# Performance work log

Measured on AMD Instinct MI355X. Metric: run time of the kernel, lower is better.

## Reference

```python
import jax, jax.numpy as jnp
import numpy as np

B, T, D = 64, 256, 512   # batch, seq_len, input_dim (= emb_dim)
HA = 512                 # alpha_dim
HB = 512                 # beta_dim (must equal alpha_dim due to source bug)
ODE = 256                # ode_dim


def _lin(key, out_d, in_d, scale):
    k1, k2 = jax.random.split(key)
    W = jax.random.uniform(k1, (out_d, in_d), jnp.float32, -scale, scale)
    b = jax.random.uniform(k2, (out_d,), jnp.float32, -scale, scale)
    return W, b


def setup_inputs() -> dict:
    key = jax.random.key(0)
    ks = jax.random.split(key, 16)
    x = jax.random.normal(ks[0], (B, T, D), jnp.float32)
    W_emb, b_emb = _lin(ks[1], D, D, 1.0 / np.sqrt(D))
    # LSTMCell params: gates order i, f, g, o ; shapes (4H, in) / (4H, H)
    sA = 1.0 / np.sqrt(HA)
    Wih_a = jax.random.uniform(ks[2], (4 * HA, D), jnp.float32, -sA, sA)
    Whh_a = jax.random.uniform(ks[3], (4 * HA, HA), jnp.float32, -sA, sA)
    bih_a = jax.random.uniform(ks[4], (4 * HA,), jnp.float32, -sA, sA)
    bhh_a = jax.random.uniform(ks[5], (4 * HA,), jnp.float32, -sA, sA)
    sB = 1.0 / np.sqrt(HB)
    Wih_b = jax.random.uniform(ks[6], (4 * HB, D), jnp.float32, -sB, sB)
    Whh_b = jax.random.uniform(ks[7], (4 * HB, HB), jnp.float32, -sB, sB)
    bih_b = jax.random.uniform(ks[8], (4 * HB,), jnp.float32, -sB, sB)
    bhh_b = jax.random.uniform(ks[9], (4 * HB,), jnp.float32, -sB, sB)
    W_aatt, b_aatt = _lin(ks[10], 1, HA, 1.0 / np.sqrt(HA))
    W_batt, b_batt = _lin(ks[11], D, HB, 1.0 / np.sqrt(HB))
    W_mu, b_mu = _lin(ks[12], ODE, D, 1.0 / np.sqrt(D))
    W_sig, b_sig = _lin(ks[13], ODE, D, 1.0 / np.sqrt(D))
    ah0 = jax.random.normal(ks[14], (B, HA), jnp.float32)
    k15a, k15b, k15c = jax.random.split(ks[15], 3)
    ac0 = jax.random.normal(k15a, (B, HA), jnp.float32)
    bh0 = jax.random.normal(k15b, (B, HB), jnp.float32)
    bc0 = jax.random.normal(k15c, (B, HB), jnp.float32)
    return dict(x=x, W_emb=W_emb, b_emb=b_emb,
                Wih_a=Wih_a, Whh_a=Whh_a, bih_a=bih_a, bhh_a=bhh_a,
                Wih_b=Wih_b, Whh_b=Whh_b, bih_b=bih_b, bhh_b=bhh_b,
                W_aatt=W_aatt, b_aatt=b_aatt, W_batt=W_batt, b_batt=b_batt,
                W_mu=W_mu, b_mu=b_mu, W_sig=W_sig, b_sig=b_sig,
                ah0=ah0, ac0=ac0, bh0=bh0, bc0=bc0)


def _lstm_scan(xs, h0, c0, Wih, Whh, bih, bhh):
    # xs: (T, B, D) -> (hs (T,B,H), hT (B,H))
    def step(carry, xt):
        h, c = carry
        g = xt @ Wih.T + bih + h @ Whh.T + bhh
        i, f, gg, o = jnp.split(g, 4, axis=-1)
        c = jax.nn.sigmoid(f) * c + jax.nn.sigmoid(i) * jnp.tanh(gg)
        h = jax.nn.sigmoid(o) * jnp.tanh(c)
        return (h, c), h
    (hT, _), hs = jax.lax.scan(step, (h0, c0), xs)
    return hs, hT


def reference(x, W_emb, b_emb, Wih_a, Whh_a, bih_a, bhh_a,
              Wih_b, Whh_b, bih_b, bhh_b, W_aatt, b_aatt,
              W_batt, b_batt, W_mu, b_mu, W_sig, b_sig,
              ah0, ac0, bh0, bc0):
    emb = x @ W_emb.T + b_emb                      # (B, T, D)
    rev = jnp.flip(emb.transpose(1, 0, 2), 0)      # (T, B, D) reversed time
    hs_a, hT_a = _lstm_scan(rev, ah0, ac0, Wih_a, Whh_a, bih_a, bhh_a)
    hi = jnp.flip(hs_a, 0).transpose(1, 0, 2)      # (B, T, HA)
    alpha = jax.nn.softmax(hi @ W_aatt.T + b_aatt, axis=1)  # (B, T, 1)
    # Faithful to source bug: beta loop appends the FINAL alpha_hx each step,
    # so gi is hT_a broadcast over time (beta LSTM output is discarded).
    _ = _lstm_scan(rev, bh0, bc0, Wih_b, Whh_b, bih_b, bhh_b)  # dead compute, DCE'd
    gi = jnp.broadcast_to(hT_a[:, None, :], (x.shape[0], x.shape[1], hT_a.shape[-1]))
    beta = jnp.tanh(gi @ W_batt.T + b_batt)        # (B, T, D)
    w = alpha * beta * emb                          # (B, T, D)
    var = jnp.sum(w, axis=1)                        # (B, D)
    mean = jnp.mean(w, axis=1)                      # (B, D)
    mu = mean @ W_mu.T + b_mu                       # (B, ODE)
    sigma = var @ W_sig.T + b_sig                   # (B, ODE)
    return (mu, sigma)
```

## Files before the change

### kernel.cpp

```cpp
#include <hip/hip_runtime.h>
#include <hip/hip_bf16.h>
#include <math.h>

#define BB_ 64
#define TT_ 256
#define DD_ 512
#define HH_ 512
#define G4_ 2048
#define ODE_ 256

#define NBLK_ 512

__device__ __forceinline__ float2 cohload2(const float* p) {
    unsigned long long u = __hip_atomic_load(
        (unsigned long long*)p, __ATOMIC_RELAXED, __HIP_MEMORY_SCOPE_AGENT);
    union { unsigned long long u; float2 f; } c; c.u = u;
    return c.f;
}
__device__ __forceinline__ void cohstore2(float* p, float a, float b) {
    union { unsigned long long u; float2 f; } c; c.f = make_float2(a, b);
    __hip_atomic_store((unsigned long long*)p, c.u,
                       __ATOMIC_RELAXED, __HIP_MEMORY_SCOPE_AGENT);
}

__device__ __forceinline__ float fsigmoid(float x) {
    return 1.f / (1.f + __expf(-x));
}
__device__ __forceinline__ float ftanh(float x) {
    float e = __expf(-2.f * fabsf(x));
    float t = (1.f - e) / (1.f + e);
    return copysignf(t, x);
}

template <int CTRL>
__device__ __forceinline__ float dpp_ror_add(float x) {
    int y = __builtin_amdgcn_update_dpp(0, __float_as_int(x), CTRL, 0xf, 0xf, false);
    return x + __int_as_float(y);
}
__device__ __forceinline__ float row16_allreduce(float x) {
    x = dpp_ror_add<0x121>(x);
    x = dpp_ror_add<0x122>(x);
    x = dpp_ror_add<0x124>(x);
    x = dpp_ror_add<0x128>(x);
    return x;
}

template <int ACT>
__global__ __launch_bounds__(256) void gemm_bt(
    const float* __restrict__ A, const float* __restrict__ W,
    const float* __restrict__ bias1, const float* __restrict__ bias2,
    float* __restrict__ C, int M, int N, int K, float scale)
{
    const int BM = 128, BN = 128, BK = 16;
    __shared__ float As[BK][BM + 4];
    __shared__ float Ws[BK][BN + 4];
    const int tid = threadIdx.x;
    const int tx = tid & 15, ty = tid >> 4;
    const int m0 = blockIdx.y * BM, n0 = blockIdx.x * BN;

    float acc[8][8];
#pragma unroll
    for (int i = 0; i < 8; ++i)
#pragma unroll
        for (int j = 0; j < 8; ++j) acc[i][j] = 0.f;

    int r0_ = (tid * 4) >> 4,        c0_ = (tid * 4) & 15;
    int r1_ = ((256 + tid) * 4) >> 4, c1_ = ((256 + tid) * 4) & 15;
    int gm0 = m0 + r0_; if (gm0 > M - 1) gm0 = M - 1;
    int gm1 = m0 + r1_; if (gm1 > M - 1) gm1 = M - 1;

    float4 pa0 = *(const float4*)(A + (size_t)gm0 * K + c0_);
    float4 pw0 = *(const float4*)(W + (size_t)(n0 + r0_) * K + c0_);
    float4 pa1 = *(const float4*)(A + (size_t)gm1 * K + c1_);
    float4 pw1 = *(const float4*)(W + (size_t)(n0 + r1_) * K + c1_);

    for (int k0 = 0; k0 < K; k0 += BK) {
        As[c0_ + 0][r0_] = pa0.x; As[c0_ + 1][r0_] = pa0.y;
        As[c0_ + 2][r0_] = pa0.z; As[c0_ + 3][r0_] = pa0.w;
        Ws[c0_ + 0][r0_] = pw0.x; Ws[c0_ + 1][r0_] = pw0.y;
        Ws[c0_ + 2][r0_] = pw0.z; Ws[c0_ + 3][r0_] = pw0.w;
        As[c1_ + 0][r1_] = pa1.x; As[c1_ + 1][r1_] = pa1.y;
        As[c1_ + 2][r1_] = pa1.z; As[c1_ + 3][r1_] = pa1.w;
        Ws[c1_ + 0][r1_] = pw1.x; Ws[c1_ + 1][r1_] = pw1.y;
        Ws[c1_ + 2][r1_] = pw1.z; Ws[c1_ + 3][r1_] = pw1.w;
        __syncthreads();

        if (k0 + BK < K) {
            int kn = k0 + BK;
            pa0 = *(const float4*)(A + (size_t)gm0 * K + kn + c0_);
            pw0 = *(const float4*)(W + (size_t)(n0 + r0_) * K + kn + c0_);
            pa1 = *(const float4*)(A + (size_t)gm1 * K + kn + c1_);
            pw1 = *(const float4*)(W + (size_t)(n0 + r1_) * K + kn + c1_);
        }

#pragma unroll
        for (int k = 0; k < BK; ++k) {
            float a[8], w[8];
#pragma unroll
            for (int i = 0; i < 8; ++i) a[i] = As[k][ty * 8 + i];
#pragma unroll
            for (int j = 0; j < 8; ++j) w[j] = Ws[k][tx * 8 + j];
#pragma unroll
            for (int i = 0; i < 8; ++i)
#pragma unroll
                for (int j = 0; j < 8; ++j) acc[i][j] += a[i] * w[j];
        }
        __syncthreads();
    }

#pragma unroll
    for (int j = 0; j < 8; ++j) {
        int n = n0 + tx * 8 + j;
        float bsum = bias1[n] + (bias2 ? bias2[n] : 0.f);
#pragma unroll
        for (int i = 0; i < 8; ++i) {
            int m = m0 + ty * 8 + i;
            if (m < M) {
                float v = acc[i][j] * scale + bsum;
                if (ACT == 1) v = tanhf(v);
                C[(size_t)m * N + n] = v;
            }
        }
    }
}

__global__ __launch_bounds__(256, 2) void lstm_persist(
    const float* __restrict__ gx,
    const float* __restrict__ Whh,
    const float* __restrict__ ac0,
    float* __restrict__ hT0,
    float* __restrict__ hT1,
    float* __restrict__ hsT,
    unsigned* __restrict__ cnt)
{
    __shared__ float h_s[512 * 12];
    __shared__ float gx_s[4 * 65];

    const int tid = threadIdx.x;
    const int bg = blockIdx.x >> 5;
    const int jb = blockIdx.x & 31;
    const int jh0 = jb * 16;
    const int b0  = bg * 4;
    const int kq   = tid & 15;
    const int jh_l = tid >> 4;
    const int jh   = jh0 + jh_l;

    float creg = 0.f;
    if (kq < 4) creg = ac0[(size_t)(b0 + kq) * HH_ + jh];

    float4 wreg[32];
#pragma unroll
    for (int kk = 0; kk < 32; ++kk) {
        int k = kk * 16 + kq;
        wreg[kk].x = Whh[(size_t)(0 * 512 + jh) * 512 + k];
        wreg[kk].y = Whh[(size_t)(1 * 512 + jh) * 512 + k];
        wreg[kk].z = Whh[(size_t)(2 * 512 + jh) * 512 + k];
        wreg[kk].w = Whh[(size_t)(3 * 512 + jh) * 512 + k];
    }

    const int g_lb = tid >> 6;
    const int g_g  = (tid >> 4) & 3;
    const int g_jl = tid & 15;
    const float* gsrc = gx + (size_t)(b0 + g_lb) * TT_ * G4_ + g_g * 512 + jh0 + g_jl;

    float gxreg = gsrc[(size_t)255 * G4_];

    for (int t = 0; t < TT_; ++t) {
        const float* hin = ((t & 1) ? hT1 : hT0) + (size_t)bg * 2048;
        float* hout      = ((t & 1) ? hT0 : hT1) + (size_t)bg * 2048;

        gx_s[g_lb * 65 + g_g * 16 + g_jl] = gxreg;

        float4 hstg[2];
#pragma unroll
        for (int w = 0; w < 2; ++w) {
            int c = w * 256 + tid;
            float2 a  = cohload2(hin + (size_t)c * 4);
            float2 b2 = cohload2(hin + (size_t)c * 4 + 2);
            hstg[w] = make_float4(a.x, a.y, b2.x, b2.y);
        }
#pragma unroll
        for (int w = 0; w < 2; ++w) {
            int c = w * 256 + tid;
            *(float4*)(h_s + (size_t)c * 12) = hstg[w];
        }
        __syncthreads();

        if (t + 1 < TT_)
            gxreg = gsrc[(size_t)(TT_ - 2 - t) * G4_];

        float acc[4][4];
#pragma unroll
        for (int i = 0; i < 4; ++i)
#pragma unroll
            for (int j = 0; j < 4; ++j) acc[i][j] = 0.f;

#pragma unroll
        for (int kk = 0; kk < 32; ++kk) {
            int k = kk * 16 + kq;
            float4 wv = wreg[kk];
            float4 ha = *(const float4*)(h_s + (size_t)k * 12);
            float hv[4] = {ha.x, ha.y, ha.z, ha.w};
#pragma unroll
            for (int bb = 0; bb < 4; ++bb) {
                acc[bb][0] += hv[bb] * wv.x;
                acc[bb][1] += hv[bb] * wv.y;
                acc[bb][2] += hv[bb] * wv.z;
                acc[bb][3] += hv[bb] * wv.w;
            }
        }

#pragma unroll
        for (int bb = 0; bb < 4; ++bb)
#pragma unroll
            for (int g = 0; g < 4; ++g)
                acc[bb][g] = row16_allreduce(acc[bb][g]);

        float hn = 0.f;
        if (kq < 4) {
            float gi = 0.f, gf = 0.f, gg = 0.f, go = 0.f;
#pragma unroll
            for (int bb = 0; bb < 4; ++bb)
                if (kq == bb) { gi = acc[bb][0]; gf = acc[bb][1];
                                gg = acc[bb][2]; go = acc[bb][3]; }
            gi += gx_s[kq * 65 + 0 * 16 + jh_l];
            gf += gx_s[kq * 65 + 1 * 16 + jh_l];
            gg += gx_s[kq * 65 + 2 * 16 + jh_l];
            go += gx_s[kq * 65 + 3 * 16 + jh_l];
            float si = fsigmoid(gi);
            float sf = fsigmoid(gf);
            float sg = ftanh(gg);
            float so = fsigmoid(go);
            creg = sf * creg + si * sg;
            hn = so * ftanh(creg);
        }
        float hn_up = __shfl_down(hn, 1);
        const bool do_st = (kq < 4) && ((kq & 1) == 0);
        if (do_st)
            cohstore2(hout + (size_t)jh * 4 + kq, hn, hn_up);

        __syncthreads();
        if (tid == 0)
            __hip_atomic_fetch_add(&cnt[(size_t)bg * 32], 1u,
                                   __ATOMIC_RELAXED, __HIP_MEMORY_SCOPE_AGENT);
        if (do_st)
            *(float2*)(hsT + ((size_t)t * 512 + jh) * 64 + b0 + kq) = make_float2(hn, hn_up);
        if (tid == 0) {
            unsigned tgt = (unsigned)(t + 1) * 32u;
            while (__hip_atomic_load(&cnt[(size_t)bg * 32],
                        __ATOMIC_RELAXED, __HIP_MEMORY_SCOPE_AGENT) < tgt)
                __builtin_amdgcn_s_sleep(1);
        }
        __syncthreads();
    }
}

__global__ __launch_bounds__(256) void h0_transpose(
    const float* __restrict__ ah0, float* __restrict__ hT0)
{
    int idx = blockIdx.x * 256 + threadIdx.x;
    int b = idx >> 9, jh = idx & 511;
    hT0[(size_t)(b >> 2) * 2048 + jh * 4 + (b & 3)] = ah0[idx];
}

__global__ __launch_bounds__(256) void att_scores_T(
    const float* __restrict__ hsT, const float* __restrict__ Wa,
    const float* __restrict__ ba, float* __restrict__ scores)
{
    int ts = blockIdx.x;
    int b = threadIdx.x & 63, part = threadIdx.x >> 6;
    const float* hp = hsT + (size_t)ts * 512 * 64;
    float s = 0.f;
#pragma unroll 8
    for (int jj = 0; jj < 128; ++jj) {
        int jh = part * 128 + jj;
        s += hp[(size_t)jh * 64 + b] * Wa[jh];
    }
    __shared__ float red[4][64];
    red[part][b] = s;
    __syncthreads();
    if (part == 0) {
        float tot = red[0][b] + red[1][b] + red[2][b] + red[3][b] + ba[0];
        scores[b * TT_ + (TT_ - 1 - ts)] = tot;
    }
}

__global__ __launch_bounds__(256) void softmax_wsum(
    const float* __restrict__ scores, const float* __restrict__ emb,
    float* __restrict__ s)
{
    const int b = blockIdx.x;
    const int tid = threadIdx.x;
    __shared__ float sm[256];
    __shared__ float red[16];
    float v = scores[b * TT_ + tid];
    float m = v;
#pragma unroll
    for (int off = 32; off; off >>= 1) m = fmaxf(m, __shfl_xor(m, off));
    int wv = tid >> 6, ln = tid & 63;
    if (ln == 0) red[wv] = m;
    __syncthreads();
    float bm = fmaxf(fmaxf(red[0], red[1]), fmaxf(red[2], red[3]));
    float e = expf(v - bm);
    float ss = e;
#pragma unroll
    for (int off = 32; off; off >>= 1) ss += __shfl_xor(ss, off);
    if (ln == 0) red[8 + wv] = ss;
    __syncthreads();
    float tot = red[8] + red[9] + red[10] + red[11];
    sm[tid] = e / tot;
    __syncthreads();

    float acc0 = 0.f, acc1 = 0.f;
    const float* ep = emb + (size_t)b * TT_ * DD_;
    for (int t = 0; t < TT_; ++t) {
        float a = sm[t];
        acc0 += a * ep[t * DD_ + tid];
        acc1 += a * ep[t * DD_ + 256 + tid];
    }
    s[b * DD_ + tid] = acc0;
    s[b * DD_ + 256 + tid] = acc1;
}

__global__ __launch_bounds__(256) void beta_from_hT(
    const float* __restrict__ hTT, const float* __restrict__ Wb,
    const float* __restrict__ bbias, float* __restrict__ beta)
{
    int b = threadIdx.x & 63, w = threadIdx.x >> 6;
    int d = blockIdx.x * 4 + w;
    const float* wrow = Wb + (size_t)d * 512;
    const float* hb = hTT + (size_t)(b >> 2) * 2048 + (b & 3);
    float s = 0.f;
#pragma unroll 8
    for (int jh = 0; jh < 512; ++jh)
        s += hb[(size_t)jh * 4] * wrow[jh];
    beta[(size_t)b * 512 + d] = tanhf(s + bbias[d]);
}

__global__ __launch_bounds__(256) void mulvec(
    const float* __restrict__ a, const float* __restrict__ b,
    float* __restrict__ o, int n)
{
    int i = blockIdx.x * 256 + threadIdx.x;
    if (i < n) o[i] = a[i] * b[i];
}

extern "C" void kernel_launch(void* const* d_in, const int* in_sizes, int n_in,
                              void* d_out, int out_size, void* d_ws, size_t ws_size,
                              hipStream_t stream) {
    const float* x      = (const float*)d_in[0];
    const float* W_emb  = (const float*)d_in[1];
    const float* b_emb  = (const float*)d_in[2];
    const float* Wih_a  = (const float*)d_in[3];
    const float* Whh_a  = (const float*)d_in[4];
    const float* bih_a  = (const float*)d_in[5];
    const float* bhh_a  = (const float*)d_in[6];
    const float* W_aatt = (const float*)d_in[11];
    const float* b_aatt = (const float*)d_in[12];
    const float* W_batt = (const float*)d_in[13];
    const float* b_batt = (const float*)d_in[14];
    const float* W_mu   = (const float*)d_in[15];
    const float* b_mu   = (const float*)d_in[16];
    const float* W_sig  = (const float*)d_in[17];
    const float* b_sig  = (const float*)d_in[18];
    const float* ah0    = (const float*)d_in[19];
    const float* ac0    = (const float*)d_in[20];

    const size_t N_EMB = (size_t)BB_ * TT_ * DD_;
    const size_t N_GX  = (size_t)BB_ * TT_ * G4_;
    const size_t N_HS  = (size_t)TT_ * HH_ * BB_;
    const size_t N_BH  = (size_t)BB_ * HH_;
    const size_t N_BAR = 8192;

    size_t need_floats = N_BAR + N_EMB + N_GX + N_HS + 2 * N_BH
                       + (size_t)BB_ * TT_ + 3 * N_BH;
    if (ws_size < need_floats * sizeof(float)) return;

    float* ws     = (float*)d_ws;
    unsigned* cnt = (unsigned*)d_ws;
    float* emb    = ws + N_BAR;
    float* gx     = emb + N_EMB;
    float* hsT    = gx + N_GX;
    float* hT0    = hsT + N_HS;
    float* hT1    = hT0 + N_BH;
    float* scores = hT1 + N_BH;
    float* svec   = scores + (size_t)BB_ * TT_;
    float* beta   = svec + N_BH;
    float* var    = beta + N_BH;

    float* out_mu  = (float*)d_out;
    float* out_sig = out_mu + (size_t)BB_ * ODE_;

    hipMemsetAsync(d_ws, 0, N_BAR * sizeof(float), stream);

    h0_transpose<<<dim3(128), dim3(256), 0, stream>>>(ah0, hT0);

    gemm_bt<0><<<dim3(DD_ / 128, (BB_ * TT_) / 128), dim3(256), 0, stream>>>(
        x, W_emb, b_emb, nullptr, emb, BB_ * TT_, DD_, DD_, 1.f);

    gemm_bt<0><<<dim3(G4_ / 128, (BB_ * TT_) / 128), dim3(256), 0, stream>>>(
        emb, Wih_a, bih_a, bhh_a, gx, BB_ * TT_, G4_, DD_, 1.f);

    lstm_persist<<<dim3(NBLK_), dim3(256), 0, stream>>>(
        gx, Whh_a, ac0, hT0, hT1, hsT, cnt);

    att_scores_T<<<dim3(TT_), dim3(256), 0, stream>>>(hsT, W_aatt, b_aatt, scores);

    softmax_wsum<<<dim3(BB_), dim3(256), 0, stream>>>(scores, emb, svec);

    beta_from_hT<<<dim3(DD_ / 4), dim3(256), 0, stream>>>(hT0, W_batt, b_batt, beta);

    mulvec<<<dim3(N_BH / 256), dim3(256), 0, stream>>>(beta, svec, var, (int)N_BH);

    gemm_bt<0><<<dim3(ODE_ / 128, 1), dim3(256), 0, stream>>>(
        var, W_mu, b_mu, nullptr, out_mu, BB_, ODE_, DD_, 1.f / 256.f);
    gemm_bt<0><<<dim3(ODE_ / 128, 1), dim3(256), 0, stream>>>(
        var, W_sig, b_sig, nullptr, out_sig, BB_, ODE_, DD_, 1.f);
}
```

Measured before the change: 1.687 ms.

## Split persistent LSTM into 2-batch groups across twice as many blocks

The persistent LSTM kernel now handles 2 batch rows per block group instead of 4, doubling the grid to 1024 blocks and raising launch bounds to 4 blocks per CU. The hidden-state exchange buffers, the h0 transpose and the beta kernel indexing are updated for the 2-wide interleaved layout. The aim is to halve the per-step FMA work in each block and shorten each step of the sequential recurrence. In exchange, Whh must sit in registers in twice as many blocks, occupancy pressure rises because the 128 weight registers per thread are unchanged, and there are more groups spinning on the barrier counters.

```diff
diff --git a/kernel.cpp b/kernel.cpp
--- a/kernel.cpp
+++ b/kernel.cpp
@@ -9,7 +9,7 @@
 #define G4_ 2048
 #define ODE_ 256
 
-#define NBLK_ 512
+#define NBLK_ 1024
 
 __device__ __forceinline__ float2 cohload2(const float* p) {
     unsigned long long u = __hip_atomic_load(
@@ -124,7 +124,7 @@
     }
 }
 
-__global__ __launch_bounds__(256, 2) void lstm_persist(
+__global__ __launch_bounds__(256, 4) void lstm_persist(
     const float* __restrict__ gx,
     const float* __restrict__ Whh,
     const float* __restrict__ ac0,
@@ -133,20 +133,20 @@
     float* __restrict__ hsT,
     unsigned* __restrict__ cnt)
 {
-    __shared__ float h_s[512 * 12];
-    __shared__ float gx_s[4 * 65];
+    __shared__ float h_s[512 * 2];
+    __shared__ float gx_s[2 * 65];
 
     const int tid = threadIdx.x;
     const int bg = blockIdx.x >> 5;
     const int jb = blockIdx.x & 31;
     const int jh0 = jb * 16;
-    const int b0  = bg * 4;
+    const int b0  = bg * 2;
     const int kq   = tid & 15;
     const int jh_l = tid >> 4;
     const int jh   = jh0 + jh_l;
 
     float creg = 0.f;
-    if (kq < 4) creg = ac0[(size_t)(b0 + kq) * HH_ + jh];
+    if (kq < 2) creg = ac0[(size_t)(b0 + kq) * HH_ + jh];
 
     float4 wreg[32];
 #pragma unroll
@@ -161,37 +161,31 @@
     const int g_lb = tid >> 6;
     const int g_g  = (tid >> 4) & 3;
     const int g_jl = tid & 15;
-    const float* gsrc = gx + (size_t)(b0 + g_lb) * TT_ * G4_ + g_g * 512 + jh0 + g_jl;
-
-    float gxreg = gsrc[(size_t)255 * G4_];
+    const bool g_act = tid < 128;
+    const float* gsrc = gx + (size_t)(b0 + (g_act ? g_lb : 0)) * TT_ * G4_
+                      + g_g * 512 + jh0 + g_jl;
+
+    float gxreg = g_act ? gsrc[(size_t)255 * G4_] : 0.f;
 
     for (int t = 0; t < TT_; ++t) {
-        const float* hin = ((t & 1) ? hT1 : hT0) + (size_t)bg * 2048;
-        float* hout      = ((t & 1) ? hT0 : hT1) + (size_t)bg * 2048;
-
-        gx_s[g_lb * 65 + g_g * 16 + g_jl] = gxreg;
-
-        float4 hstg[2];
-#pragma unroll
-        for (int w = 0; w < 2; ++w) {
-            int c = w * 256 + tid;
-            float2 a  = cohload2(hin + (size_t)c * 4);
-            float2 b2 = cohload2(hin + (size_t)c * 4 + 2);
-            hstg[w] = make_float4(a.x, a.y, b2.x, b2.y);
-        }
-#pragma unroll
-        for (int w = 0; w < 2; ++w) {
-            int c = w * 256 + tid;
-            *(float4*)(h_s + (size_t)c * 12) = hstg[w];
+        const float* hin = ((t & 1) ? hT1 : hT0) + (size_t)bg * 1024;
+        float* hout      = ((t & 1) ? hT0 : hT1) + (size_t)bg * 1024;
+
+        if (g_act) gx_s[g_lb * 65 + g_g * 16 + g_jl] = gxreg;
+
+        {
+            float2 a  = cohload2(hin + (size_t)tid * 4);
+            float2 b2 = cohload2(hin + (size_t)tid * 4 + 2);
+            *(float4*)(h_s + (size_t)tid * 4) = make_float4(a.x, a.y, b2.x, b2.y);
         }
         __syncthreads();
 
-        if (t + 1 < TT_)
+        if (g_act && t + 1 < TT_)
             gxreg = gsrc[(size_t)(TT_ - 2 - t) * G4_];
 
-        float acc[4][4];
-#pragma unroll
-        for (int i = 0; i < 4; ++i)
+        float acc[2][4];
+#pragma unroll
+        for (int i = 0; i < 2; ++i)
 #pragma unroll
             for (int j = 0; j < 4; ++j) acc[i][j] = 0.f;
 
@@ -199,10 +193,10 @@
         for (int kk = 0; kk < 32; ++kk) {
             int k = kk * 16 + kq;
             float4 wv = wreg[kk];
-            float4 ha = *(const float4*)(h_s + (size_t)k * 12);
-            float hv[4] = {ha.x, ha.y, ha.z, ha.w};
-#pragma unroll
-            for (int bb = 0; bb < 4; ++bb) {
+            float2 ha = *(const float2*)(h_s + (size_t)k * 2);
+            float hv[2] = {ha.x, ha.y};
+#pragma unroll
+            for (int bb = 0; bb < 2; ++bb) {
                 acc[bb][0] += hv[bb] * wv.x;
                 acc[bb][1] += hv[bb] * wv.y;
                 acc[bb][2] += hv[bb] * wv.z;
@@ -211,16 +205,16 @@
         }
 
 #pragma unroll
-        for (int bb = 0; bb < 4; ++bb)
+        for (int bb = 0; bb < 2; ++bb)
 #pragma unroll
             for (int g = 0; g < 4; ++g)
                 acc[bb][g] = row16_allreduce(acc[bb][g]);
 
         float hn = 0.f;
-        if (kq < 4) {
+        if (kq < 2) {
             float gi = 0.f, gf = 0.f, gg = 0.f, go = 0.f;
 #pragma unroll
-            for (int bb = 0; bb < 4; ++bb)
+            for (int bb = 0; bb < 2; ++bb)
                 if (kq == bb) { gi = acc[bb][0]; gf = acc[bb][1];
                                 gg = acc[bb][2]; go = acc[bb][3]; }
             gi += gx_s[kq * 65 + 0 * 16 + jh_l];
@@ -235,16 +229,16 @@
             hn = so * ftanh(creg);
         }
         float hn_up = __shfl_down(hn, 1);
-        const bool do_st = (kq < 4) && ((kq & 1) == 0);
+        const bool do_st = (kq == 0);
         if (do_st)
-            cohstore2(hout + (size_t)jh * 4 + kq, hn, hn_up);
+            cohstore2(hout + (size_t)jh * 2, hn, hn_up);
 
         __syncthreads();
         if (tid == 0)
             __hip_atomic_fetch_add(&cnt[(size_t)bg * 32], 1u,
                                    __ATOMIC_RELAXED, __HIP_MEMORY_SCOPE_AGENT);
         if (do_st)
-            *(float2*)(hsT + ((size_t)t * 512 + jh) * 64 + b0 + kq) = make_float2(hn, hn_up);
+            *(float2*)(hsT + ((size_t)t * 512 + jh) * 64 + b0) = make_float2(hn, hn_up);
         if (tid == 0) {
             unsigned tgt = (unsigned)(t + 1) * 32u;
             while (__hip_atomic_load(&cnt[(size_t)bg * 32],
@@ -260,7 +254,7 @@
 {
     int idx = blockIdx.x * 256 + threadIdx.x;
     int b = idx >> 9, jh = idx & 511;
-    hT0[(size_t)(b >> 2) * 2048 + jh * 4 + (b & 3)] = ah0[idx];
+    hT0[(size_t)(b >> 1) * 1024 + jh * 2 + (b & 1)] = ah0[idx];
 }
 
 __global__ __launch_bounds__(256) void att_scores_T(
@@ -329,11 +323,11 @@
     int b = threadIdx.x & 63, w = threadIdx.x >> 6;
     int d = blockIdx.x * 4 + w;
     const float* wrow = Wb + (size_t)d * 512;
-    const float* hb = hTT + (size_t)(b >> 2) * 2048 + (b & 3);
+    const float* hb = hTT + (size_t)(b >> 1) * 1024 + (b & 1);
     float s = 0.f;
 #pragma unroll 8
     for (int jh = 0; jh < 512; ++jh)
-        s += hb[(size_t)jh * 4] * wrow[jh];
+        s += hb[(size_t)jh * 2] * wrow[jh];
     beta[(size_t)b * 512 + d] = tanhf(s + bbias[d]);
 }
 
```

After: 3.282 ms. 94.5% more time.

## Fuse attention tail into one kernel and add release flag to LSTM barrier

Applied to the files above, without the earlier changes.

Replaces the softmax/weighted-sum, beta projection, elementwise multiply and two output GEMMs with one per-batch kernel that computes beta, the product and the mu/sigma projections from shared memory. It also changes the LSTM inter-block barrier so the last arriving block writes a separate per-group flag, and waiters poll that flag instead of the contended counter. This removes four launches and intermediate global buffers, and cuts polling traffic on the atomic counter. The cost is that each of 64 blocks rereads the W_batt, W_mu and W_sig matrices from memory.

```diff
diff --git a/kernel.cpp b/kernel.cpp
--- a/kernel.cpp
+++ b/kernel.cpp
@@ -240,15 +240,18 @@
             cohstore2(hout + (size_t)jh * 4 + kq, hn, hn_up);
 
         __syncthreads();
-        if (tid == 0)
-            __hip_atomic_fetch_add(&cnt[(size_t)bg * 32], 1u,
+        if (tid == 0) {
+            unsigned old = __hip_atomic_fetch_add(&cnt[(size_t)bg * 32], 1u,
                                    __ATOMIC_RELAXED, __HIP_MEMORY_SCOPE_AGENT);
+            if (old == (unsigned)(t + 1) * 32u - 1u)
+                __hip_atomic_store(&cnt[2048 + (size_t)bg * 32], (unsigned)(t + 1),
+                                   __ATOMIC_RELAXED, __HIP_MEMORY_SCOPE_AGENT);
+        }
         if (do_st)
             *(float2*)(hsT + ((size_t)t * 512 + jh) * 64 + b0 + kq) = make_float2(hn, hn_up);
         if (tid == 0) {
-            unsigned tgt = (unsigned)(t + 1) * 32u;
-            while (__hip_atomic_load(&cnt[(size_t)bg * 32],
-                        __ATOMIC_RELAXED, __HIP_MEMORY_SCOPE_AGENT) < tgt)
+            while (__hip_atomic_load(&cnt[2048 + (size_t)bg * 32],
+                        __ATOMIC_RELAXED, __HIP_MEMORY_SCOPE_AGENT) < (unsigned)(t + 1))
                 __builtin_amdgcn_s_sleep(1);
         }
         __syncthreads();
@@ -285,20 +288,30 @@
     }
 }
 
-__global__ __launch_bounds__(256) void softmax_wsum(
-    const float* __restrict__ scores, const float* __restrict__ emb,
-    float* __restrict__ s)
+__global__ __launch_bounds__(256) void fused_tail(
+    const float* __restrict__ scores,
+    const float* __restrict__ emb,
+    const float* __restrict__ hTT,
+    const float* __restrict__ W_batt, const float* __restrict__ b_batt,
+    const float* __restrict__ W_mu,   const float* __restrict__ b_mu,
+    const float* __restrict__ W_sig,  const float* __restrict__ b_sig,
+    float* __restrict__ out_mu, float* __restrict__ out_sig)
 {
     const int b = blockIdx.x;
     const int tid = threadIdx.x;
+    const int wv = tid >> 6, ln = tid & 63;
     __shared__ float sm[256];
+    __shared__ float sv_s[512];
+    __shared__ float hT_s[512];
     __shared__ float red[16];
+
     float v = scores[b * TT_ + tid];
     float m = v;
 #pragma unroll
     for (int off = 32; off; off >>= 1) m = fmaxf(m, __shfl_xor(m, off));
-    int wv = tid >> 6, ln = tid & 63;
     if (ln == 0) red[wv] = m;
+    hT_s[tid]       = hTT[(size_t)(b >> 2) * 2048 + (size_t)tid * 4 + (b & 3)];
+    hT_s[tid + 256] = hTT[(size_t)(b >> 2) * 2048 + (size_t)(tid + 256) * 4 + (b & 3)];
     __syncthreads();
     float bm = fmaxf(fmaxf(red[0], red[1]), fmaxf(red[2], red[3]));
     float e = expf(v - bm);
@@ -318,31 +331,36 @@
         acc0 += a * ep[t * DD_ + tid];
         acc1 += a * ep[t * DD_ + 256 + tid];
     }
-    s[b * DD_ + tid] = acc0;
-    s[b * DD_ + 256 + tid] = acc1;
-}
-
-__global__ __launch_bounds__(256) void beta_from_hT(
-    const float* __restrict__ hTT, const float* __restrict__ Wb,
-    const float* __restrict__ bbias, float* __restrict__ beta)
-{
-    int b = threadIdx.x & 63, w = threadIdx.x >> 6;
-    int d = blockIdx.x * 4 + w;
-    const float* wrow = Wb + (size_t)d * 512;
-    const float* hb = hTT + (size_t)(b >> 2) * 2048 + (b & 3);
-    float s = 0.f;
-#pragma unroll 8
-    for (int jh = 0; jh < 512; ++jh)
-        s += hb[(size_t)jh * 4] * wrow[jh];
-    beta[(size_t)b * 512 + d] = tanhf(s + bbias[d]);
-}
-
-__global__ __launch_bounds__(256) void mulvec(
-    const float* __restrict__ a, const float* __restrict__ b,
-    float* __restrict__ o, int n)
-{
-    int i = blockIdx.x * 256 + threadIdx.x;
-    if (i < n) o[i] = a[i] * b[i];
+    sv_s[tid] = acc0;
+    sv_s[tid + 256] = acc1;
+    __syncthreads();
+
+    for (int i = 0; i < 128; ++i) {
+        int d = wv * 128 + i;
+        const float* wr = W_batt + (size_t)d * 512;
+        float s = 0.f;
+#pragma unroll
+        for (int q = 0; q < 8; ++q) s += wr[ln + q * 64] * hT_s[ln + q * 64];
+#pragma unroll
+        for (int off = 32; off; off >>= 1) s += __shfl_xor(s, off);
+        if (ln == 0) sv_s[d] = ftanh(s + b_batt[d]) * sv_s[d];
+    }
+    __syncthreads();
+
+    for (int i = 0; i < 128; ++i) {
+        int o = wv * 128 + i;
+        const float* wr = (o < 256) ? (W_mu + (size_t)o * 512)
+                                    : (W_sig + (size_t)(o - 256) * 512);
+        float s = 0.f;
+#pragma unroll
+        for (int q = 0; q < 8; ++q) s += wr[ln + q * 64] * sv_s[ln + q * 64];
+#pragma unroll
+        for (int off = 32; off; off >>= 1) s += __shfl_xor(s, off);
+        if (ln == 0) {
+            if (o < 256) out_mu[(size_t)b * ODE_ + o] = s * (1.f / 256.f) + b_mu[o];
+            else         out_sig[(size_t)b * ODE_ + (o - 256)] = s + b_sig[o - 256];
+        }
+    }
 }
 
 extern "C" void kernel_launch(void* const* d_in, const int* in_sizes, int n_in,
@@ -384,9 +402,6 @@
     float* hT0    = hsT + N_HS;
     float* hT1    = hT0 + N_BH;
     float* scores = hT1 + N_BH;
-    float* svec   = scores + (size_t)BB_ * TT_;
-    float* beta   = svec + N_BH;
-    float* var    = beta + N_BH;
 
     float* out_mu  = (float*)d_out;
     float* out_sig = out_mu + (size_t)BB_ * ODE_;
@@ -406,14 +421,7 @@
 
     att_scores_T<<<dim3(TT_), dim3(256), 0, stream>>>(hsT, W_aatt, b_aatt, scores);
 
-    softmax_wsum<<<dim3(BB_), dim3(256), 0, stream>>>(scores, emb, svec);
-
-    beta_from_hT<<<dim3(DD_ / 4), dim3(256), 0, stream>>>(hT0, W_batt, b_batt, beta);
-
-    mulvec<<<dim3(N_BH / 256), dim3(256), 0, stream>>>(beta, svec, var, (int)N_BH);
-
-    gemm_bt<0><<<dim3(ODE_ / 128, 1), dim3(256), 0, stream>>>(
-        var, W_mu, b_mu, nullptr, out_mu, BB_, ODE_, DD_, 1.f / 256.f);
-    gemm_bt<0><<<dim3(ODE_ / 128, 1), dim3(256), 0, stream>>>(
-        var, W_sig, b_sig, nullptr, out_sig, BB_, ODE_, DD_, 1.f);
-}
+    fused_tail<<<dim3(BB_), dim3(256), 0, stream>>>(
+        scores, emb, hT0, W_batt, b_batt, W_mu, b_mu, W_sig, b_sig,
+        out_mu, out_sig);
+}
```

After: 1.581 ms. 1.07x faster.
